# Performance work log

Measured on AMD Instinct MI355X. Metric: run time of the kernel, lower is better.

Reference implementation:

```python
import jax, jax.numpy as jnp
import numpy as np
from jax.ops import segment_sum

NUM_HEADS = 16
NEG_INF = -jnp.inf


def setup_inputs() -> dict:
    key = jax.random.key(0)
    ks = jax.random.split(key, 12)
    D, H = 1024, NUM_HEADS
    SRC, TGT = 2048, 2048
    V, EV = 32000, 2000
    s = 1.0 / np.sqrt(D)
    return {
        "logits": jax.random.normal(ks[0], (TGT, V), jnp.float32),
        "extended_vocab_ids": jax.random.randint(ks[1], (SRC,), 0, V + EV, jnp.int32),
        "src_subtokens": jax.random.normal(ks[2], (SRC, D), jnp.float32),
        "tgt_subtokens": jax.random.normal(ks[3], (TGT, D), jnp.float32),
        "w_q": jax.random.normal(ks[4], (D, D), jnp.float32) * s,
        "b_q": jax.random.normal(ks[5], (D,), jnp.float32) * 0.02,
        "w_k": jax.random.normal(ks[6], (D, D), jnp.float32) * s,
        "b_k": jax.random.normal(ks[7], (D,), jnp.float32) * 0.02,
        "w_ptr": jax.random.normal(ks[8], (D,), jnp.float32) * s,
        "b_ptr": jax.random.normal(ks[9], (1,), jnp.float32) * 0.02,
        "len_vocab": V,
        "len_extended_vocab": EV,
    }


def _mha_attention(query, key, w_q, b_q, w_k, b_k):
    # SimpleMHA.unbatched_forward: project q/k, per-head scaled dot-product
    # softmax over src, mean over heads -> [TGT, SRC]
    TGT, D = query.shape
    SRC = key.shape[0]
    hd = D // NUM_HEADS
    q = (query @ w_q.T + b_q).reshape(TGT, NUM_HEADS, hd)
    k = (key @ w_k.T + b_k).reshape(SRC, NUM_HEADS, hd)
    scores = jnp.einsum("thd,shd->hts", q, k) / jnp.sqrt(jnp.float32(hd))
    attn = jax.nn.softmax(scores, axis=-1)  # [H, TGT, SRC]
    return attn.mean(axis=0)  # [TGT, SRC]


def reference(logits, extended_vocab_ids, src_subtokens, tgt_subtokens,
              w_q, b_q, w_k, b_k, w_ptr, b_ptr, len_vocab, len_extended_vocab):
    total = len_vocab + len_extended_vocab
    eps = jnp.finfo(jnp.float32).eps
    fmin = jnp.finfo(jnp.float32).min

    # copy gate: sigmoid(Linear(tgt)) -> [TGT, 1]
    copy_prob = jax.nn.sigmoid(tgt_subtokens @ w_ptr + b_ptr[0])[:, None]

    # attention distribution over src tokens [TGT, SRC]
    attn = _mha_attention(tgt_subtokens, src_subtokens, w_q, b_q, w_k, b_k)

    # attention @ one-hot(M) == scatter-add of attention columns by vocab id
    attn_vocab = segment_sum(attn.T, extended_vocab_ids, num_segments=total).T  # [TGT, total]
    attn_vocab = jnp.where(attn_vocab == 0, eps, attn_vocab)
    pointer_log_probs = jnp.log(attn_vocab)

    decoder_log_probs = jax.nn.log_softmax(logits, axis=1)
    decoder_log_probs = jnp.pad(decoder_log_probs, ((0, 0), (0, len_extended_vocab)),
                                constant_values=NEG_INF)

    p = jnp.stack([decoder_log_probs + jnp.log(1.0 - copy_prob),
                   pointer_log_probs + jnp.log(copy_prob)])
    p = jnp.where(p == NEG_INF, fmin, p)
    return jax.scipy.special.logsumexp(p, axis=0)
```

## Files before the change

kernel.cpp:

```cpp
#include <hip/hip_runtime.h>

typedef __attribute__((ext_vector_type(8))) short short8;
typedef __attribute__((ext_vector_type(4))) float f32x4;
typedef __attribute__((ext_vector_type(4))) unsigned int u32x4;
typedef unsigned short u16;
typedef unsigned int u32;

#define MFMA16 __builtin_amdgcn_mfma_f32_16x16x32_bf16

static constexpr int TGT = 2048, SRCN = 2048, DIM = 1024, NH = 16;
static constexpr int NV = 32000, NTOT = 34000;
#define FLT_EPS 1.1920928955078125e-07f

__device__ __forceinline__ u16 f2bf(float f) {
  unsigned u = __float_as_uint(f);
  return (u16)((u + 0x7FFFu + ((u >> 16) & 1u)) >> 16);
}

__device__ __forceinline__ int swz8(int row, int seg) {
  return row * 64 + ((seg ^ (row & 7)) << 3);
}

__device__ __forceinline__ void stats_row_body(
    int t, const float* __restrict__ logits, const float* __restrict__ tgt,
    const float* __restrict__ w_ptr, const float* __restrict__ b_ptr,
    float4* __restrict__ rowc, int tid, int lane, int w, float* red) {
  const f32x4* l4 = (const f32x4*)(logits + (size_t)t * NV);
  float e0 = 0.f, e1 = 0.f, e2 = 0.f, e3 = 0.f;
  const f32x4 z4 = {0.f, 0.f, 0.f, 0.f};
#pragma unroll 2
  for (int pk = 0; pk < 8; ++pk) {
    int g0 = pk * 1024 + tid;
    int g1 = g0 + 256, g2 = g0 + 512, g3 = g0 + 768;
    bool d0 = g0 < NV / 4, d1 = g1 < NV / 4, d2 = g2 < NV / 4, d3 = g3 < NV / 4;
    f32x4 v0 = d0 ? l4[g0] : z4;
    f32x4 v1 = d1 ? l4[g1] : z4;
    f32x4 v2 = d2 ? l4[g2] : z4;
    f32x4 v3 = d3 ? l4[g3] : z4;
    float s0 = (__expf(v0.x) + __expf(v0.y)) + (__expf(v0.z) + __expf(v0.w));
    float s1 = (__expf(v1.x) + __expf(v1.y)) + (__expf(v1.z) + __expf(v1.w));
    float s2 = (__expf(v2.x) + __expf(v2.y)) + (__expf(v2.z) + __expf(v2.w));
    float s3 = (__expf(v3.x) + __expf(v3.y)) + (__expf(v3.z) + __expf(v3.w));
    e0 += d0 ? s0 : 0.f;
    e1 += d1 ? s1 : 0.f;
    e2 += d2 ? s2 : 0.f;
    e3 += d3 ? s3 : 0.f;
  }
  float es = (e0 + e1) + (e2 + e3);

  float4 xv = *(const float4*)&tgt[(size_t)t * DIM + tid * 4];
  float4 wv = *(const float4*)&w_ptr[tid * 4];
  float g = (xv.x * wv.x + xv.y * wv.y) + (xv.z * wv.z + xv.w * wv.w);
  for (int d = 1; d < 64; d <<= 1) {
    es += __shfl_xor(es, d, 64);
    g += __shfl_xor(g, d, 64);
  }
  if (lane == 0) { red[w] = es; red[4 + w] = g; }
  __syncthreads();
  if (tid == 0) {
    float tot = red[0] + red[1] + red[2] + red[3];
    float gs = red[4] + red[5] + red[6] + red[7] + b_ptr[0];
    float c = 1.0f / (1.0f + __expf(-gs));
    float4 rc;
    rc.x = (1.0f - c) / tot;
    rc.y = c * FLT_EPS;
    rc.z = c;
    rc.w = 0.f;
    rowc[t] = rc;
  }
}

__device__ __forceinline__ void sort_body(
    const int* __restrict__ ids, int* __restrict__ sperm,
    u32* __restrict__ segmap, u32* __restrict__ ustart,
    int tid, int lane, int w, char* smem) {
  int* kk_ = (int*)smem;
  int* vv_ = (int*)(smem + 8192);
  for (int i = tid; i < 2048; i += 256) { kk_[i] = ids[i]; vv_[i] = i; }
  for (int i = tid; i < 2048; i += 256) ustart[i] = 0xFFFFFFFFu;
  __syncthreads();
  for (int kk = 2; kk <= 2048; kk <<= 1)
    for (int j = kk >> 1; j > 0; j >>= 1) {
      for (int m = tid; m < 1024; m += 256) {
        int i = ((m & ~(j - 1)) << 1) | (m & (j - 1));
        int l = i | j;
        bool asc = ((i & kk) == 0);
        int ki = kk_[i], kl = kk_[l];
        if ((ki > kl) == asc) {
          kk_[i] = kl; kk_[l] = ki;
          int tv = vv_[i]; vv_[i] = vv_[l]; vv_[l] = tv;
        }
      }
      __syncthreads();
    }
  for (int i = tid; i < 2048; i += 256) sperm[i] = vv_[i];
  for (int i = tid; i < NTOT; i += 256) segmap[i] = 0xFFFFFFFFu;
  __syncthreads();
  int* scan = vv_;
  if (tid == 0) scan[4] = 0;
  __syncthreads();
  for (int c = 0; c < 8; ++c) {
    int p = c * 256 + tid;
    int id = kk_[p];
    bool head = (p == 0) || (kk_[p - 1] != id);
    unsigned long long bal = __ballot(head);
    int lanepfx = __popcll(bal & ((1ull << lane) - 1ull));
    int wtot = __popcll(bal);
    if (lane == 0) scan[w] = wtot;
    __syncthreads();
    int woff = 0;
    for (int i = 0; i < w; ++i) woff += scan[i];
    int base = scan[4];
    if (head) {
      int q = p + 1;
      while (q < 2048 && kk_[q] == id) ++q;
      int rank = base + woff + lanepfx;
      u32 cnt = (u32)(q - p);
      segmap[id] = (u32)rank | (cnt << 16);
      ustart[rank] = (u32)p | (cnt << 16);
    }
    __syncthreads();
    if (tid == 0) scan[4] = base + scan[0] + scan[1] + scan[2] + scan[3];
    __syncthreads();
  }
}

__device__ __forceinline__ void proj_body(
    int bb, const float* __restrict__ Xq, const float* __restrict__ Wq,
    const float* __restrict__ Bq, u16* __restrict__ Cq,
    const float* __restrict__ Xk, const float* __restrict__ Wk,
    const float* __restrict__ Bk, u16* __restrict__ Ck,
    int tid, int lane, int w, char* smem) {
  const int zz = bb >> 7;
  const float* X = zz ? Xk : Xq;
  const float* W = zz ? Wk : Wq;
  const float* bias = zz ? Bk : Bq;
  u16* C = zz ? Ck : Cq;
  const float scale = zz ? 1.0f : 0.125f;

  u16* As = (u16*)smem;
  u16* Bs = (u16*)(smem + 8192);
  const int n0 = (bb & 7) * 128, m0 = ((bb >> 3) & 15) * 128;
  const int wr = w >> 1, wc = w & 1;
  const int srow = tid >> 1, shalf = tid & 1;
  f32x4 acc[4][4] = {};

  for (int k0 = 0; k0 < DIM; k0 += 32) {
    __syncthreads();
    {
      const float* pa = X + (size_t)(m0 + srow) * DIM + k0 + shalf * 16;
      const float* pb = W + (size_t)(n0 + srow) * DIM + k0 + shalf * 16;
      float4 a0 = ((const float4*)pa)[0], a1 = ((const float4*)pa)[1];
      float4 a2 = ((const float4*)pa)[2], a3 = ((const float4*)pa)[3];
      float4 b0 = ((const float4*)pb)[0], b1 = ((const float4*)pb)[1];
      float4 b2 = ((const float4*)pb)[2], b3 = ((const float4*)pb)[3];
      short8 wa0, wa1, wb0, wb1;
      wa0[0]=(short)f2bf(a0.x); wa0[1]=(short)f2bf(a0.y); wa0[2]=(short)f2bf(a0.z); wa0[3]=(short)f2bf(a0.w);
      wa0[4]=(short)f2bf(a1.x); wa0[5]=(short)f2bf(a1.y); wa0[6]=(short)f2bf(a1.z); wa0[7]=(short)f2bf(a1.w);
      wa1[0]=(short)f2bf(a2.x); wa1[1]=(short)f2bf(a2.y); wa1[2]=(short)f2bf(a2.z); wa1[3]=(short)f2bf(a2.w);
      wa1[4]=(short)f2bf(a3.x); wa1[5]=(short)f2bf(a3.y); wa1[6]=(short)f2bf(a3.z); wa1[7]=(short)f2bf(a3.w);
      wb0[0]=(short)f2bf(b0.x); wb0[1]=(short)f2bf(b0.y); wb0[2]=(short)f2bf(b0.z); wb0[3]=(short)f2bf(b0.w);
      wb0[4]=(short)f2bf(b1.x); wb0[5]=(short)f2bf(b1.y); wb0[6]=(short)f2bf(b1.z); wb0[7]=(short)f2bf(b1.w);
      wb1[0]=(short)f2bf(b2.x); wb1[1]=(short)f2bf(b2.y); wb1[2]=(short)f2bf(b2.z); wb1[3]=(short)f2bf(b2.w);
      wb1[4]=(short)f2bf(b3.x); wb1[5]=(short)f2bf(b3.y); wb1[6]=(short)f2bf(b3.z); wb1[7]=(short)f2bf(b3.w);
      int swz = (srow >> 1) & 3;
      int sg0 = ((shalf * 2 + 0) ^ swz) << 3;
      int sg1 = ((shalf * 2 + 1) ^ swz) << 3;
      *(short8*)&As[srow * 32 + sg0] = wa0;
      *(short8*)&As[srow * 32 + sg1] = wa1;
      *(short8*)&Bs[srow * 32 + sg0] = wb0;
      *(short8*)&Bs[srow * 32 + sg1] = wb1;
    }
    __syncthreads();
    const int kq = lane >> 4;
    short8 af[4], bfr[4];
    for (int f = 0; f < 4; ++f) {
      int ar = wr * 64 + f * 16 + (lane & 15);
      af[f] = *(const short8*)&As[ar * 32 + ((kq ^ ((ar >> 1) & 3)) << 3)];
      int br = wc * 64 + f * 16 + (lane & 15);
      bfr[f] = *(const short8*)&Bs[br * 32 + ((kq ^ ((br >> 1) & 3)) << 3)];
    }
    for (int fr = 0; fr < 4; ++fr)
      for (int fc = 0; fc < 4; ++fc)
        acc[fr][fc] = MFMA16(af[fr], bfr[fc], acc[fr][fc], 0, 0, 0);
  }

  for (int fc = 0; fc < 4; ++fc) {
    int col = n0 + wc * 64 + fc * 16 + (lane & 15);
    float bv = bias[col];
    for (int fr = 0; fr < 4; ++fr)
      for (int r = 0; r < 4; ++r) {
        int rowm = m0 + wr * 64 + fr * 16 + ((lane >> 4) << 2) + r;
        C[(size_t)rowm * DIM + col] = f2bf((acc[fr][fc][r] + bv) * scale);
      }
  }
}

__global__ __launch_bounds__(256) void fused_a_kernel(
    const float* __restrict__ logits, const float* __restrict__ tgt,
    const float* __restrict__ src,
    const float* __restrict__ w_q, const float* __restrict__ b_q,
    const float* __restrict__ w_k, const float* __restrict__ b_k,
    const float* __restrict__ w_ptr, const float* __restrict__ b_ptr,
    const int* __restrict__ ids,
    u16* __restrict__ Qb, u16* __restrict__ Kb,
    int* __restrict__ sperm, u32* __restrict__ segmap,
    u32* __restrict__ ustart, float4* __restrict__ rowc) {
  __shared__ __align__(16) char smem[16384];
  const int b = blockIdx.x;
  const int tid = threadIdx.x, lane = tid & 63, w = tid >> 6;

  if (b < 256) {
    proj_body(b, tgt, w_q, b_q, Qb, src, w_k, b_k, Kb, tid, lane, w, smem);
  } else if (b == 256) {
    sort_body(ids, sperm, segmap, ustart, tid, lane, w, smem);
  } else {
    stats_row_body(b - 257, logits, tgt, w_ptr, b_ptr, rowc, tid, lane, w, (float*)smem);
  }
}

__global__ __launch_bounds__(256) void zsum_kernel(const u16* __restrict__ Qb,
                                                   const u16* __restrict__ Kb,
                                                   float* __restrict__ Zinv) {
  __shared__ u16 Ks[64 * 64];
  const int h = blockIdx.x, t0 = blockIdx.y * 64;
  const int tid = threadIdx.x, lane = tid & 63, w = tid >> 6;
  const int arow = t0 + w * 16 + (lane & 15);
  const int acol = h * 64 + ((lane >> 4) << 3);
  short8 a0 = *(const short8*)&Qb[(size_t)arow * DIM + acol];
  short8 a1 = *(const short8*)&Qb[(size_t)arow * DIM + acol + 32];
  float zacc[4] = {0.f, 0.f, 0.f, 0.f};

  for (int s0 = 0; s0 < SRCN; s0 += 64) {
    __syncthreads();
    for (int q = tid; q < 512; q += 256) {
      int r = q >> 3, seg = q & 7;
      *(short8*)&Ks[swz8(r, seg)] = *(const short8*)&Kb[(size_t)(s0 + r) * DIM + h * 64 + seg * 8];
    }
    __syncthreads();
    for (int sub = 0; sub < 4; ++sub) {
      int brow = sub * 16 + (lane & 15);
      int slo = (lane >> 4);
      short8 b0 = *(const short8*)&Ks[swz8(brow, slo)];
      short8 b1 = *(const short8*)&Ks[swz8(brow, slo + 4)];
      f32x4 c = {0.f, 0.f, 0.f, 0.f};
      c = MFMA16(a0, b0, c, 0, 0, 0);
      c = MFMA16(a1, b1, c, 0, 0, 0);
      zacc[0] += __expf(c[0]); zacc[1] += __expf(c[1]);
      zacc[2] += __expf(c[2]); zacc[3] += __expf(c[3]);
    }
  }
  for (int d = 1; d < 16; d <<= 1) {
    zacc[0] += __shfl_xor(zacc[0], d, 64);
    zacc[1] += __shfl_xor(zacc[1], d, 64);
    zacc[2] += __shfl_xor(zacc[2], d, 64);
    zacc[3] += __shfl_xor(zacc[3], d, 64);
  }
  if ((lane & 15) == 0) {
    int trow = t0 + w * 16 + ((lane >> 4) << 2);
    for (int r = 0; r < 4; ++r)
      Zinv[h * TGT + trow + r] = 1.0f / (16.0f * zacc[r]);
  }
}

__global__ __launch_bounds__(256) void attn_kernel(
    const u16* __restrict__ Qb, const u16* __restrict__ Kb,
    const float* __restrict__ Zinv, float* __restrict__ attn) {
  __shared__ __align__(16) char smem[16384];
  u16* Qs = (u16*)smem;
  u16* Ks = (u16*)(smem + 8192);
  const int bb = blockIdx.x;
  const int s0 = (bb & 31) * 64, t0 = (bb >> 5) * 64;
  const int tid = threadIdx.x, lane = tid & 63, w = tid >> 6;
  const int wr = w >> 1, wc = w & 1;
  f32x4 acc[2][2] = {};

  for (int h = 0; h < NH; ++h) {
    __syncthreads();
    for (int q = tid; q < 512; q += 256) {
      int r = q >> 3, seg = q & 7;
      *(short8*)&Qs[swz8(r, seg)] = *(const short8*)&Qb[(size_t)(t0 + r) * DIM + h * 64 + seg * 8];
      *(short8*)&Ks[swz8(r, seg)] = *(const short8*)&Kb[(size_t)(s0 + r) * DIM + h * 64 + seg * 8];
    }
    __syncthreads();
    f32x4 sc[2][2] = {};
    for (int kk = 0; kk < 2; ++kk) {
      int seg = (lane >> 4) + kk * 4;
      short8 a0 = *(const short8*)&Qs[swz8(wr * 32 + (lane & 15), seg)];
      short8 a1 = *(const short8*)&Qs[swz8(wr * 32 + 16 + (lane & 15), seg)];
      short8 b0 = *(const short8*)&Ks[swz8(wc * 32 + (lane & 15), seg)];
      short8 b1 = *(const short8*)&Ks[swz8(wc * 32 + 16 + (lane & 15), seg)];
      sc[0][0] = MFMA16(a0, b0, sc[0][0], 0, 0, 0);
      sc[0][1] = MFMA16(a0, b1, sc[0][1], 0, 0, 0);
      sc[1][0] = MFMA16(a1, b0, sc[1][0], 0, 0, 0);
      sc[1][1] = MFMA16(a1, b1, sc[1][1], 0, 0, 0);
    }
    for (int fr = 0; fr < 2; ++fr) {
      int trow = t0 + wr * 32 + fr * 16 + ((lane >> 4) << 2);
      float4 z4 = *(const float4*)&Zinv[h * TGT + trow];
      float iz[4] = {z4.x, z4.y, z4.z, z4.w};
      for (int fc = 0; fc < 2; ++fc)
        for (int r = 0; r < 4; ++r)
          acc[fr][fc][r] += __expf(sc[fr][fc][r]) * iz[r];
    }
  }
  for (int fr = 0; fr < 2; ++fr)
    for (int fc = 0; fc < 2; ++fc)
      for (int r = 0; r < 4; ++r) {
        int t = t0 + wr * 32 + fr * 16 + ((lane >> 4) << 2) + r;
        int s = s0 + wc * 32 + fc * 16 + (lane & 15);
        attn[(size_t)t * SRCN + s] = acc[fr][fc][r];
      }
}

__global__ __launch_bounds__(512) void out_kernel(
    const float* __restrict__ logits, const float4* __restrict__ rowc,
    const int* __restrict__ sperm, const u32* __restrict__ segmap,
    const u32* __restrict__ ustart, const float* __restrict__ attn,
    float* __restrict__ out) {
  __shared__ float aL[2048];
  __shared__ float pL[2048];
  const int t = (TGT - 1) - blockIdx.x;
  const int tid = threadIdx.x;
  float4 rc = rowc[t];
  const float K1 = rc.x, Ceps = rc.y, cc = rc.z;
  const f32x4* l4 = (const f32x4*)(logits + (size_t)t * NV);
  f32x4* o4 = (f32x4*)(out + (size_t)t * NTOT);
  const u32x4* m4 = (const u32x4*)segmap;

  *(float4*)&aL[tid * 4] = *(const float4*)&attn[(size_t)t * SRCN + tid * 4];
  __syncthreads();
  for (int r = tid; r < 2048; r += 512) {
    u32 u = ustart[r];
    if (u != 0xFFFFFFFFu) {
      int p = (int)(u & 0xFFFFu), n = (int)(u >> 16);
      float s = 0.f;
      for (int k = 0; k < n; ++k) s += aL[sperm[p + k]];
      pL[r] = cc * s;
    }
  }
  __syncthreads();

  auto psum = [&](u32 mv) -> float {
    return (mv == 0xFFFFFFFFu) ? Ceps : pL[mv & 0xFFFFu];
  };
  auto elem = [&](float v, bool d, u32 mv) -> float {
    float e = d ? __expf(v) : 0.f;
    return __logf(fmaf(e, K1, psum(mv)));
  };

  const f32x4 z4 = {0.f, 0.f, 0.f, 0.f};
#pragma unroll
  for (int pk = 0; pk < 4; ++pk) {
    int g0 = pk * 2048 + tid;
    int g1 = g0 + 512, g2 = g0 + 1024, g3 = g0 + 1536;
    u32x4 m0 = m4[g0], m1 = m4[g1], m2 = m4[g2], m3 = m4[g3];
    bool d0 = g0 < NV / 4, d1 = g1 < NV / 4, d2 = g2 < NV / 4, d3 = g3 < NV / 4;
    f32x4 v0 = d0 ? __builtin_nontemporal_load(&l4[g0]) : z4;
    f32x4 v1 = d1 ? __builtin_nontemporal_load(&l4[g1]) : z4;
    f32x4 v2 = d2 ? __builtin_nontemporal_load(&l4[g2]) : z4;
    f32x4 v3 = d3 ? __builtin_nontemporal_load(&l4[g3]) : z4;
    f32x4 o0, o1, o2, o3;
    o0.x = elem(v0.x, d0, m0.x); o0.y = elem(v0.y, d0, m0.y);
    o0.z = elem(v0.z, d0, m0.z); o0.w = elem(v0.w, d0, m0.w);
    o1.x = elem(v1.x, d1, m1.x); o1.y = elem(v1.y, d1, m1.y);
    o1.z = elem(v1.z, d1, m1.z); o1.w = elem(v1.w, d1, m1.w);
    o2.x = elem(v2.x, d2, m2.x); o2.y = elem(v2.y, d2, m2.y);
    o2.z = elem(v2.z, d2, m2.z); o2.w = elem(v2.w, d2, m2.w);
    o3.x = elem(v3.x, d3, m3.x); o3.y = elem(v3.y, d3, m3.y);
    o3.z = elem(v3.z, d3, m3.z); o3.w = elem(v3.w, d3, m3.w);
    __builtin_nontemporal_store(o0, &o4[g0]);
    __builtin_nontemporal_store(o1, &o4[g1]);
    __builtin_nontemporal_store(o2, &o4[g2]);
    __builtin_nontemporal_store(o3, &o4[g3]);
  }
  for (int g = 8192 + tid; g < NTOT / 4; g += 512) {
    u32x4 m = m4[g];
    f32x4 o;
    o.x = __logf(psum(m.x));
    o.y = __logf(psum(m.y));
    o.z = __logf(psum(m.z));
    o.w = __logf(psum(m.w));
    __builtin_nontemporal_store(o, &o4[g]);
  }
}

extern "C" void kernel_launch(void* const* d_in, const int* in_sizes, int n_in,
                              void* d_out, int out_size, void* d_ws, size_t ws_size,
                              hipStream_t stream) {
  const float* logits = (const float*)d_in[0];
  const int* ids      = (const int*)d_in[1];
  const float* src    = (const float*)d_in[2];
  const float* tgt    = (const float*)d_in[3];
  const float* w_q    = (const float*)d_in[4];
  const float* b_q    = (const float*)d_in[5];
  const float* w_k    = (const float*)d_in[6];
  const float* b_k    = (const float*)d_in[7];
  const float* w_ptr  = (const float*)d_in[8];
  const float* b_ptr  = (const float*)d_in[9];
  float* out = (float*)d_out;

  char* ws = (char*)d_ws;
  u16* Qb     = (u16*)(ws);
  u16* Kb     = (u16*)(ws + (size_t)4 * 1024 * 1024);
  float* Zinv = (float*)(ws + (size_t)8 * 1024 * 1024);
  float* attn = (float*)(ws + (size_t)8 * 1024 * 1024 + 131072);
  size_t tail_off = (size_t)8 * 1024 * 1024 + 131072 + (size_t)16 * 1024 * 1024;
  int* sperm   = (int*)(ws + tail_off);
  u32* segmap  = (u32*)(ws + tail_off + 8192);
  u32* ustart  = (u32*)(ws + tail_off + 8192 + 136000);
  float4* rowc = (float4*)(ws + tail_off + 8192 + 136000 + 8192);

  fused_a_kernel<<<2305, 256, 0, stream>>>(logits, tgt, src, w_q, b_q, w_k, b_k,
                                           w_ptr, b_ptr, ids, Qb, Kb,
                                           sperm, segmap, ustart, rowc);
  zsum_kernel<<<dim3(16, 32), 256, 0, stream>>>(Qb, Kb, Zinv);
  attn_kernel<<<1024, 256, 0, stream>>>(Qb, Kb, Zinv, attn);
  out_kernel<<<TGT, 512, 0, stream>>>(logits, rowc, sperm, segmap, ustart, attn, out);
}
```

Baseline: 225.5 us.

## Split logits row-stats work across projection and zsum kernels for load balance

The per-row logits statistics blocks are split: the first 896 rows stay in the projection kernel, and the remaining rows move into a new fused kernel that also runs the softmax-denominator (zsum) blocks. The aim is to pair the memory-bound logits reduction with the compute-bound projection and zsum phases, so each kernel has a better mix of work and less tail imbalance. The cost is a fixed split ratio that may not match the actual phase durations, plus a larger shared-memory footprint for the zsum blocks.

```diff
diff --git a/kernel.cpp b/kernel.cpp
--- a/kernel.cpp
+++ b/kernel.cpp
@@ -10,6 +10,7 @@
 
 static constexpr int TGT = 2048, SRCN = 2048, DIM = 1024, NH = 16;
 static constexpr int NV = 32000, NTOT = 34000;
+static constexpr int STATS_A = 896;
 #define FLT_EPS 1.1920928955078125e-07f
 
 __device__ __forceinline__ u16 f2bf(float f) {
@@ -196,6 +197,49 @@
   }
 }
 
+__device__ __forceinline__ void zsum_body(
+    int bb, const u16* __restrict__ Qb, const u16* __restrict__ Kb,
+    float* __restrict__ Zinv, int tid, int lane, int w, char* smem) {
+  u16* Ks = (u16*)smem;
+  const int h = bb & 15, t0 = (bb >> 4) * 64;
+  const int arow = t0 + w * 16 + (lane & 15);
+  const int acol = h * 64 + ((lane >> 4) << 3);
+  short8 a0 = *(const short8*)&Qb[(size_t)arow * DIM + acol];
+  short8 a1 = *(const short8*)&Qb[(size_t)arow * DIM + acol + 32];
+  float zacc[4] = {0.f, 0.f, 0.f, 0.f};
+
+  for (int s0 = 0; s0 < SRCN; s0 += 64) {
+    __syncthreads();
+    for (int q = tid; q < 512; q += 256) {
+      int r = q >> 3, seg = q & 7;
+      *(short8*)&Ks[swz8(r, seg)] = *(const short8*)&Kb[(size_t)(s0 + r) * DIM + h * 64 + seg * 8];
+    }
+    __syncthreads();
+    for (int sub = 0; sub < 4; ++sub) {
+      int brow = sub * 16 + (lane & 15);
+      int slo = (lane >> 4);
+      short8 b0 = *(const short8*)&Ks[swz8(brow, slo)];
+      short8 b1 = *(const short8*)&Ks[swz8(brow, slo + 4)];
+      f32x4 c = {0.f, 0.f, 0.f, 0.f};
+      c = MFMA16(a0, b0, c, 0, 0, 0);
+      c = MFMA16(a1, b1, c, 0, 0, 0);
+      zacc[0] += __expf(c[0]); zacc[1] += __expf(c[1]);
+      zacc[2] += __expf(c[2]); zacc[3] += __expf(c[3]);
+    }
+  }
+  for (int d = 1; d < 16; d <<= 1) {
+    zacc[0] += __shfl_xor(zacc[0], d, 64);
+    zacc[1] += __shfl_xor(zacc[1], d, 64);
+    zacc[2] += __shfl_xor(zacc[2], d, 64);
+    zacc[3] += __shfl_xor(zacc[3], d, 64);
+  }
+  if ((lane & 15) == 0) {
+    int trow = t0 + w * 16 + ((lane >> 4) << 2);
+    for (int r = 0; r < 4; ++r)
+      Zinv[h * TGT + trow + r] = 1.0f / (16.0f * zacc[r]);
+  }
+}
+
 __global__ __launch_bounds__(256) void fused_a_kernel(
     const float* __restrict__ logits, const float* __restrict__ tgt,
     const float* __restrict__ src,
@@ -219,47 +263,21 @@
   }
 }
 
-__global__ __launch_bounds__(256) void zsum_kernel(const u16* __restrict__ Qb,
-                                                   const u16* __restrict__ Kb,
-                                                   float* __restrict__ Zinv) {
-  __shared__ u16 Ks[64 * 64];
-  const int h = blockIdx.x, t0 = blockIdx.y * 64;
+__global__ __launch_bounds__(256) void fused_b_kernel(
+    const u16* __restrict__ Qb, const u16* __restrict__ Kb,
+    float* __restrict__ Zinv,
+    const float* __restrict__ logits, const float* __restrict__ tgt,
+    const float* __restrict__ w_ptr, const float* __restrict__ b_ptr,
+    float4* __restrict__ rowc) {
+  __shared__ __align__(16) char smem[16384];
+  const int b = blockIdx.x;
   const int tid = threadIdx.x, lane = tid & 63, w = tid >> 6;
-  const int arow = t0 + w * 16 + (lane & 15);
-  const int acol = h * 64 + ((lane >> 4) << 3);
-  short8 a0 = *(const short8*)&Qb[(size_t)arow * DIM + acol];
-  short8 a1 = *(const short8*)&Qb[(size_t)arow * DIM + acol + 32];
-  float zacc[4] = {0.f, 0.f, 0.f, 0.f};
-
-  for (int s0 = 0; s0 < SRCN; s0 += 64) {
-    __syncthreads();
-    for (int q = tid; q < 512; q += 256) {
-      int r = q >> 3, seg = q & 7;
-      *(short8*)&Ks[swz8(r, seg)] = *(const short8*)&Kb[(size_t)(s0 + r) * DIM + h * 64 + seg * 8];
-    }
-    __syncthreads();
-    for (int sub = 0; sub < 4; ++sub) {
-      int brow = sub * 16 + (lane & 15);
-      int slo = (lane >> 4);
-      short8 b0 = *(const short8*)&Ks[swz8(brow, slo)];
-      short8 b1 = *(const short8*)&Ks[swz8(brow, slo + 4)];
-      f32x4 c = {0.f, 0.f, 0.f, 0.f};
-      c = MFMA16(a0, b0, c, 0, 0, 0);
-      c = MFMA16(a1, b1, c, 0, 0, 0);
-      zacc[0] += __expf(c[0]); zacc[1] += __expf(c[1]);
-      zacc[2] += __expf(c[2]); zacc[3] += __expf(c[3]);
-    }
-  }
-  for (int d = 1; d < 16; d <<= 1) {
-    zacc[0] += __shfl_xor(zacc[0], d, 64);
-    zacc[1] += __shfl_xor(zacc[1], d, 64);
-    zacc[2] += __shfl_xor(zacc[2], d, 64);
-    zacc[3] += __shfl_xor(zacc[3], d, 64);
-  }
-  if ((lane & 15) == 0) {
-    int trow = t0 + w * 16 + ((lane >> 4) << 2);
-    for (int r = 0; r < 4; ++r)
-      Zinv[h * TGT + trow + r] = 1.0f / (16.0f * zacc[r]);
+
+  if (b < 512) {
+    zsum_body(b, Qb, Kb, Zinv, tid, lane, w, smem);
+  } else {
+    stats_row_body(STATS_A + (b - 512), logits, tgt, w_ptr, b_ptr, rowc,
+                   tid, lane, w, (float*)smem);
   }
 }
 
@@ -411,10 +429,11 @@
   u32* ustart  = (u32*)(ws + tail_off + 8192 + 136000);
   float4* rowc = (float4*)(ws + tail_off + 8192 + 136000 + 8192);
 
-  fused_a_kernel<<<2305, 256, 0, stream>>>(logits, tgt, src, w_q, b_q, w_k, b_k,
-                                           w_ptr, b_ptr, ids, Qb, Kb,
-                                           sperm, segmap, ustart, rowc);
-  zsum_kernel<<<dim3(16, 32), 256, 0, stream>>>(Qb, Kb, Zinv);
+  fused_a_kernel<<<257 + STATS_A, 256, 0, stream>>>(logits, tgt, src, w_q, b_q,
+                                                    w_k, b_k, w_ptr, b_ptr, ids,
+                                                    Qb, Kb, sperm, segmap, ustart, rowc);
+  fused_b_kernel<<<512 + (TGT - STATS_A), 256, 0, stream>>>(Qb, Kb, Zinv, logits,
+                                                            tgt, w_ptr, b_ptr, rowc);
   attn_kernel<<<1024, 256, 0, stream>>>(Qb, Kb, Zinv, attn);
   out_kernel<<<TGT, 512, 0, stream>>>(logits, rowc, sperm, segmap, ustart, attn, out);
 }
```

New measurement: 237.8 us. +5.5%, slower.

## Cache exp(logits) as bf16 in stats pass and reuse in output kernel

Applied to the files above, without the earlier changes.

The stats pass now stores exp(logits) as bf16 into workspace, and a new output kernel reads these halves instead of re-reading fp32 logits and recomputing exp. The aim is to cut the second pass's read bandwidth and exp work. In exchange it adds a bf16 write in the first pass and loses precision in the decoder probability term. It only runs when the workspace is large enough.

```diff
diff --git a/kernel.cpp b/kernel.cpp
--- a/kernel.cpp
+++ b/kernel.cpp
@@ -1,6 +1,7 @@
 #include <hip/hip_runtime.h>
 
 typedef __attribute__((ext_vector_type(8))) short short8;
+typedef __attribute__((ext_vector_type(8))) unsigned short u16x8;
 typedef __attribute__((ext_vector_type(4))) float f32x4;
 typedef __attribute__((ext_vector_type(4))) unsigned int u32x4;
 typedef unsigned short u16;
@@ -16,6 +17,9 @@
   unsigned u = __float_as_uint(f);
   return (u16)((u + 0x7FFFu + ((u >> 16) & 1u)) >> 16);
 }
+__device__ __forceinline__ float bf2f(u16 h) {
+  return __uint_as_float(((unsigned)h) << 16);
+}
 
 __device__ __forceinline__ int swz8(int row, int seg) {
   return row * 64 + ((seg ^ (row & 7)) << 3);
@@ -24,9 +28,11 @@
 __device__ __forceinline__ void stats_row_body(
     int t, const float* __restrict__ logits, const float* __restrict__ tgt,
     const float* __restrict__ w_ptr, const float* __restrict__ b_ptr,
-    float4* __restrict__ rowc, int tid, int lane, int w, float* red) {
+    float4* __restrict__ rowc, u16* __restrict__ expb,
+    int tid, int lane, int w, float* red) {
   const f32x4* l4 = (const f32x4*)(logits + (size_t)t * NV);
-  float e0 = 0.f, e1 = 0.f, e2 = 0.f, e3 = 0.f;
+  u16* erow = expb ? expb + (size_t)t * NV : (u16*)0;
+  float a0 = 0.f, a1 = 0.f, a2 = 0.f, a3 = 0.f;
   const f32x4 z4 = {0.f, 0.f, 0.f, 0.f};
 #pragma unroll 2
   for (int pk = 0; pk < 8; ++pk) {
@@ -37,16 +43,23 @@
     f32x4 v1 = d1 ? l4[g1] : z4;
     f32x4 v2 = d2 ? l4[g2] : z4;
     f32x4 v3 = d3 ? l4[g3] : z4;
-    float s0 = (__expf(v0.x) + __expf(v0.y)) + (__expf(v0.z) + __expf(v0.w));
-    float s1 = (__expf(v1.x) + __expf(v1.y)) + (__expf(v1.z) + __expf(v1.w));
-    float s2 = (__expf(v2.x) + __expf(v2.y)) + (__expf(v2.z) + __expf(v2.w));
-    float s3 = (__expf(v3.x) + __expf(v3.y)) + (__expf(v3.z) + __expf(v3.w));
-    e0 += d0 ? s0 : 0.f;
-    e1 += d1 ? s1 : 0.f;
-    e2 += d2 ? s2 : 0.f;
-    e3 += d3 ? s3 : 0.f;
-  }
-  float es = (e0 + e1) + (e2 + e3);
+    f32x4 e0v, e1v, e2v, e3v;
+    e0v.x = __expf(v0.x); e0v.y = __expf(v0.y); e0v.z = __expf(v0.z); e0v.w = __expf(v0.w);
+    e1v.x = __expf(v1.x); e1v.y = __expf(v1.y); e1v.z = __expf(v1.z); e1v.w = __expf(v1.w);
+    e2v.x = __expf(v2.x); e2v.y = __expf(v2.y); e2v.z = __expf(v2.z); e2v.w = __expf(v2.w);
+    e3v.x = __expf(v3.x); e3v.y = __expf(v3.y); e3v.z = __expf(v3.z); e3v.w = __expf(v3.w);
+    if (erow) {
+      if (d0) { ushort4 p = {f2bf(e0v.x), f2bf(e0v.y), f2bf(e0v.z), f2bf(e0v.w)}; *(ushort4*)&erow[g0 * 4] = p; }
+      if (d1) { ushort4 p = {f2bf(e1v.x), f2bf(e1v.y), f2bf(e1v.z), f2bf(e1v.w)}; *(ushort4*)&erow[g1 * 4] = p; }
+      if (d2) { ushort4 p = {f2bf(e2v.x), f2bf(e2v.y), f2bf(e2v.z), f2bf(e2v.w)}; *(ushort4*)&erow[g2 * 4] = p; }
+      if (d3) { ushort4 p = {f2bf(e3v.x), f2bf(e3v.y), f2bf(e3v.z), f2bf(e3v.w)}; *(ushort4*)&erow[g3 * 4] = p; }
+    }
+    a0 += d0 ? (e0v.x + e0v.y) + (e0v.z + e0v.w) : 0.f;
+    a1 += d1 ? (e1v.x + e1v.y) + (e1v.z + e1v.w) : 0.f;
+    a2 += d2 ? (e2v.x + e2v.y) + (e2v.z + e2v.w) : 0.f;
+    a3 += d3 ? (e3v.x + e3v.y) + (e3v.z + e3v.w) : 0.f;
+  }
+  float es = (a0 + a1) + (a2 + a3);
 
   float4 xv = *(const float4*)&tgt[(size_t)t * DIM + tid * 4];
   float4 wv = *(const float4*)&w_ptr[tid * 4];
@@ -205,7 +218,8 @@
     const int* __restrict__ ids,
     u16* __restrict__ Qb, u16* __restrict__ Kb,
     int* __restrict__ sperm, u32* __restrict__ segmap,
-    u32* __restrict__ ustart, float4* __restrict__ rowc) {
+    u32* __restrict__ ustart, float4* __restrict__ rowc,
+    u16* __restrict__ expb) {
   __shared__ __align__(16) char smem[16384];
   const int b = blockIdx.x;
   const int tid = threadIdx.x, lane = tid & 63, w = tid >> 6;
@@ -215,7 +229,8 @@
   } else if (b == 256) {
     sort_body(ids, sperm, segmap, ustart, tid, lane, w, smem);
   } else {
-    stats_row_body(b - 257, logits, tgt, w_ptr, b_ptr, rowc, tid, lane, w, (float*)smem);
+    stats_row_body(b - 257, logits, tgt, w_ptr, b_ptr, rowc, expb,
+                   tid, lane, w, (float*)smem);
   }
 }
 
@@ -311,6 +326,82 @@
         int s = s0 + wc * 32 + fc * 16 + (lane & 15);
         attn[(size_t)t * SRCN + s] = acc[fr][fc][r];
       }
+}
+
+__global__ __launch_bounds__(512) void out_expb_kernel(
+    const u16* __restrict__ expb, const float4* __restrict__ rowc,
+    const int* __restrict__ sperm, const u32* __restrict__ segmap,
+    const u32* __restrict__ ustart, const float* __restrict__ attn,
+    float* __restrict__ out) {
+  __shared__ float aL[2048];
+  __shared__ float pL[2048];
+  const int t = (TGT - 1) - blockIdx.x;
+  const int tid = threadIdx.x;
+  float4 rc = rowc[t];
+  const float K1 = rc.x, Ceps = rc.y, cc = rc.z;
+  const u16x8* e8 = (const u16x8*)(expb + (size_t)t * NV);
+  f32x4* o4 = (f32x4*)(out + (size_t)t * NTOT);
+  const u32x4* m4 = (const u32x4*)segmap;
+
+  *(float4*)&aL[tid * 4] = *(const float4*)&attn[(size_t)t * SRCN + tid * 4];
+  __syncthreads();
+  for (int r = tid; r < 2048; r += 512) {
+    u32 u = ustart[r];
+    if (u != 0xFFFFFFFFu) {
+      int p = (int)(u & 0xFFFFu), n = (int)(u >> 16);
+      float s = 0.f;
+      for (int k = 0; k < n; ++k) s += aL[sperm[p + k]];
+      pL[r] = cc * s;
+    }
+  }
+  __syncthreads();
+
+  auto psum = [&](u32 mv) -> float {
+    return (mv == 0xFFFFFFFFu) ? Ceps : pL[mv & 0xFFFFu];
+  };
+
+  const u16x8 hz = {0, 0, 0, 0, 0, 0, 0, 0};
+#pragma unroll
+  for (int pk = 0; pk < 4; ++pk) {
+    const int gb = pk * 1024 + tid;
+    int gi0 = gb, gi1 = gb + 512;
+    bool d0 = gi0 < NV / 8, d1 = gi1 < NV / 8;
+    u32x4 m00 = m4[gi0 * 2], m01 = m4[gi0 * 2 + 1];
+    u32x4 m10 = m4[gi1 * 2], m11 = m4[gi1 * 2 + 1];
+    u16x8 e0 = d0 ? e8[gi0] : hz;
+    u16x8 e1 = d1 ? e8[gi1] : hz;
+    f32x4 oa, ob;
+    oa.x = __logf(fmaf(d0 ? bf2f(e0[0]) : 0.f, K1, psum(m00.x)));
+    oa.y = __logf(fmaf(d0 ? bf2f(e0[1]) : 0.f, K1, psum(m00.y)));
+    oa.z = __logf(fmaf(d0 ? bf2f(e0[2]) : 0.f, K1, psum(m00.z)));
+    oa.w = __logf(fmaf(d0 ? bf2f(e0[3]) : 0.f, K1, psum(m00.w)));
+    ob.x = __logf(fmaf(d0 ? bf2f(e0[4]) : 0.f, K1, psum(m01.x)));
+    ob.y = __logf(fmaf(d0 ? bf2f(e0[5]) : 0.f, K1, psum(m01.y)));
+    ob.z = __logf(fmaf(d0 ? bf2f(e0[6]) : 0.f, K1, psum(m01.z)));
+    ob.w = __logf(fmaf(d0 ? bf2f(e0[7]) : 0.f, K1, psum(m01.w)));
+    __builtin_nontemporal_store(oa, &o4[gi0 * 2]);
+    __builtin_nontemporal_store(ob, &o4[gi0 * 2 + 1]);
+    f32x4 oc, od;
+    oc.x = __logf(fmaf(d1 ? bf2f(e1[0]) : 0.f, K1, psum(m10.x)));
+    oc.y = __logf(fmaf(d1 ? bf2f(e1[1]) : 0.f, K1, psum(m10.y)));
+    oc.z = __logf(fmaf(d1 ? bf2f(e1[2]) : 0.f, K1, psum(m10.z)));
+    oc.w = __logf(fmaf(d1 ? bf2f(e1[3]) : 0.f, K1, psum(m10.w)));
+    od.x = __logf(fmaf(d1 ? bf2f(e1[4]) : 0.f, K1, psum(m11.x)));
+    od.y = __logf(fmaf(d1 ? bf2f(e1[5]) : 0.f, K1, psum(m11.y)));
+    od.z = __logf(fmaf(d1 ? bf2f(e1[6]) : 0.f, K1, psum(m11.z)));
+    od.w = __logf(fmaf(d1 ? bf2f(e1[7]) : 0.f, K1, psum(m11.w)));
+    __builtin_nontemporal_store(oc, &o4[gi1 * 2]);
+    __builtin_nontemporal_store(od, &o4[gi1 * 2 + 1]);
+  }
+  for (int g = 8000 + tid; g < NTOT / 4; g += 512) {
+    u32x4 m = m4[g];
+    f32x4 o;
+    o.x = __logf(psum(m.x));
+    o.y = __logf(psum(m.y));
+    o.z = __logf(psum(m.z));
+    o.w = __logf(psum(m.w));
+    __builtin_nontemporal_store(o, &o4[g]);
+  }
 }
 
 __global__ __launch_bounds__(512) void out_kernel(
@@ -410,11 +501,18 @@
   u32* segmap  = (u32*)(ws + tail_off + 8192);
   u32* ustart  = (u32*)(ws + tail_off + 8192 + 136000);
   float4* rowc = (float4*)(ws + tail_off + 8192 + 136000 + 8192);
+  size_t expb_off = (tail_off + 8192 + 136000 + 8192 + 32768 + 255) & ~(size_t)255;
+  size_t expb_bytes = (size_t)TGT * NV * 2;
+  bool use_expb = ws_size >= expb_off + expb_bytes;
+  u16* expb = use_expb ? (u16*)(ws + expb_off) : (u16*)0;
 
   fused_a_kernel<<<2305, 256, 0, stream>>>(logits, tgt, src, w_q, b_q, w_k, b_k,
                                            w_ptr, b_ptr, ids, Qb, Kb,
-                                           sperm, segmap, ustart, rowc);
+                                           sperm, segmap, ustart, rowc, expb);
   zsum_kernel<<<dim3(16, 32), 256, 0, stream>>>(Qb, Kb, Zinv);
   attn_kernel<<<1024, 256, 0, stream>>>(Qb, Kb, Zinv, attn);
-  out_kernel<<<TGT, 512, 0, stream>>>(logits, rowc, sperm, segmap, ustart, attn, out);
-}
+  if (use_expb)
+    out_expb_kernel<<<TGT, 512, 0, stream>>>(expb, rowc, sperm, segmap, ustart, attn, out);
+  else
+    out_kernel<<<TGT, 512, 0, stream>>>(logits, rowc, sperm, segmap, ustart, attn, out);
+}
```

Result: slower. 255.7 us (+13.4%).
